# Kernel tuning notes

Measured on AMD Instinct MI355X. Metric: run time of the kernel, lower is better.

Reference implementation:

```python
import jax, jax.numpy as jnp
import numpy as np

B, T, D, C = 2, 2048, 1024, 10
F = D // 2 + 1  # rfft bins; permutations act on frequency bins (perm_freq=True)


def setup_inputs() -> dict:
    key = jax.random.key(0)
    ks = jax.random.split(key, 6)
    s = 1.0 / np.sqrt(D)
    x = jax.random.normal(ks[0], (B, T, D), jnp.float32)
    Wq = jax.random.normal(ks[1], (D, D), jnp.float32) * s
    Wk = jax.random.normal(ks[2], (D, D), jnp.float32) * s
    Wv = jax.random.normal(ks[3], (D, D), jnp.float32) * s
    Wo = jax.random.normal(ks[4], (D, D), jnp.float32) * s
    # buffer: torch.randn(C, F).argsort(-1) -> random permutations of freq bins
    perms = jnp.argsort(jax.random.normal(ks[5], (C, F)), axis=-1)
    return {"x": x, "Wq": Wq, "Wk": Wk, "Wv": Wv, "Wo": Wo, "perms": perms}


def reference(x, Wq, Wk, Wv, Wo, perms):
    # linear projections (nn.Linear applies x @ W.T)
    q = x @ Wq.T
    k = x @ Wk.T
    v = x @ Wv.T
    # HRR bind/unbind in rfft frequency domain
    fq = jnp.fft.rfft(q, axis=-1)  # (B,T,F) complex
    fk = jnp.fft.rfft(k, axis=-1)
    fv = jnp.fft.rfft(v, axis=-1)
    # gather permuted redundant copies of freq bins: (B,T,C,F) -> (C,B,T,F)
    fkp = jnp.moveaxis(fk[..., perms], 2, 0)
    fqp = jnp.moveaxis(fq[..., perms], 2, 0)
    # causal associative memory: cumulative sum of key*value bindings over time
    kv = jnp.cumsum(fkp * fv[None], axis=-2)  # (C,B,T,F)
    # unbind with query (circular correlation = multiply by conj), mean copies
    r = jnp.mean(kv * jnp.conj(fqp), axis=0)  # (B,T,F)
    values_hat = jnp.fft.irfft(r, n=D, axis=-1)  # (B,T,D)
    return values_hat @ Wo.T
```

## Files before the change

### kernel.cpp

```cpp
#include <hip/hip_runtime.h>
#include <math.h>

#define B_   2
#define T_   2048
#define D_   1024
#define C_   10
#define F_   513
#define NTOK (B_ * T_)
#define LF   3078
#define LFP  3136
#define KP2  1056
#define NCH  128
#define TC   (T_ / NCH)

typedef unsigned short us16;
typedef __attribute__((ext_vector_type(8))) __bf16 bf16x8;
typedef __attribute__((ext_vector_type(4))) float  f32x4;

#define O_XBF    ((size_t)0)
#define O_PREP   ((size_t)8388608)
#define O_WT     (O_PREP)
#define O_WOBF   (O_PREP + 6291456)
#define O_TCS    (O_PREP + 8388608)
#define O_RCAT   (O_PREP)
#define O_SFB    (O_PREP + 10489856)
#define O_MALLB  (O_SFB + 2162688)
#define O_MOUTB  (O_MALLB + 6303744)
#define O_FALL   (O_MOUTB + 2162688)
#define O_SSCAN  (O_FALL + 25690112)

__device__ __forceinline__ us16 f2b(float f) {
    union { float f; unsigned u; } v; v.f = f;
    unsigned r = v.u + 0x7FFFu + ((v.u >> 16) & 1u);
    return (us16)(r >> 16);
}

__device__ __forceinline__ float2 b2f2(unsigned w) {
    union { unsigned u; float f; } a, b;
    a.u = (w & 0xffffu) << 16;
    b.u = w & 0xffff0000u;
    return make_float2(a.f, b.f);
}

__device__ __forceinline__ void gl_lds16(const us16* g, us16* l) {
    __builtin_amdgcn_global_load_lds(
        (const __attribute__((address_space(1))) unsigned*)g,
        (__attribute__((address_space(3))) unsigned*)l, 16, 0, 0);
}

__global__ __launch_bounds__(256)
void hrr_prep(const float* __restrict__ x,  const float* __restrict__ Wq,
              const float* __restrict__ Wk, const float* __restrict__ Wv,
              const float* __restrict__ Wo,
              us16* __restrict__ Xbf, us16* __restrict__ WT,
              us16* __restrict__ WoBf, us16* __restrict__ Tcs,
              us16* __restrict__ Sfb) {
    __shared__ float t[32][33];
    const int bid = blockIdx.x, tid = threadIdx.x;
    if (bid < 4096) {
        int i = bid * 256 + tid;
        float4 v = ((const float4*)x)[i];
        ushort4 o;
        o.x = f2b(v.x); o.y = f2b(v.y); o.z = f2b(v.z); o.w = f2b(v.w);
        ((ushort4*)Xbf)[i] = o;
    } else if (bid < 5120) {
        int i = (bid - 4096) * 256 + tid;
        float4 v = ((const float4*)Wo)[i];
        ushort4 o;
        o.x = f2b(v.x); o.y = f2b(v.y); o.z = f2b(v.z); o.w = f2b(v.w);
        ((ushort4*)WoBf)[i] = o;
    } else if (bid < 8192) {
        const int l  = bid - 5120;
        const int bz = l >> 10, l2 = l & 1023;
        const int bx = (l2 & 31) * 32, by = (l2 >> 5) * 32;
        const float* W = (bz == 0) ? Wq : (bz == 1) ? Wk : Wv;
        us16* O = WT + (size_t)bz * D_ * D_;
        const int tx = tid & 31, ty = tid >> 5;
#pragma unroll
        for (int i = 0; i < 32; i += 8)
            t[ty + i][tx] = W[(size_t)(by + ty + i) * D_ + bx + tx];
        __syncthreads();
#pragma unroll
        for (int i = 0; i < 32; i += 8)
            O[(size_t)(bx + ty + i) * D_ + by + tx] = f2b(t[tx][ty + i]);
    } else if (bid < 12296) {
        int idx = (bid - 8192) * 256 + tid;
        int r = idx >> 10, e = idx & 1023;
        int f = r >> 1;
        float ang = (float)((f * e) & 1023) * 6.135923151542565e-3f;
        Tcs[idx] = f2b((r & 1) ? -sinf(ang) : cosf(ang));
    } else {
        int idx = (bid - 12296) * 256 + tid;
        int r = idx >> 10, e = idx & 1023;
        float v = 0.f;
        if (r < 1026) {
            int f = r >> 1;
            float s = (f == 0 || f == 512) ? (1.0f / 1024.0f) : (2.0f / 1024.0f);
            float ang = (float)((f * e) & 1023) * 6.135923151542565e-3f;
            v = (r & 1) ? -s * sinf(ang) : s * cosf(ang);
        }
        Sfb[idx] = f2b(v);
    }
}

template <bool OUT_BF16>
__device__ __forceinline__ void gemm_core(
    const us16* __restrict__ A, const us16* __restrict__ B, void* __restrict__ Cv,
    int M, int N, int K, int lda, int ldb, int ldc, int Ncap,
    int bm, int bn, us16* smem) {
    us16* As = smem;
    us16* Bs = smem + 8192;

    const int tid  = threadIdx.x;
    const int lane = tid & 63;
    const int wave = tid >> 6;
    const int wm = (wave >> 1) * 64;
    const int wn = (wave & 1) * 64;

    const int r0    = tid >> 2;
    const int g_lds = tid & 3;
    const int g_src = g_lds ^ ((r0 >> 1) & 3);
    const int c4    = g_src * 8;

    int rA0 = bm + r0;      if (rA0 >= M) rA0 = M - 1;
    int rA1 = bm + 64 + r0; if (rA1 >= M) rA1 = M - 1;
    int rB0 = bn + r0;      if (rB0 >= N) rB0 = N - 1;
    int rB1 = bn + 64 + r0; if (rB1 >= N) rB1 = N - 1;
    const us16* pA0 = A + (size_t)rA0 * lda + c4;
    const us16* pA1 = A + (size_t)rA1 * lda + c4;
    const us16* pB0 = B + (size_t)rB0 * ldb + c4;
    const us16* pB1 = B + (size_t)rB1 * ldb + c4;

    f32x4 acc[4][4];
#pragma unroll
    for (int i = 0; i < 4; i++)
#pragma unroll
        for (int j = 0; j < 4; j++) acc[i][j] = (f32x4){0.f, 0.f, 0.f, 0.f};

    const int fr = lane & 15;
    const int gq = ((lane >> 4) ^ ((fr >> 1) & 3)) * 8;

    const int wb = wave * 512;
#define STAGE_TILE(buf, ko)                                  \
    do {                                                     \
        us16* a_ = As + (buf) * 4096 + wb;                   \
        us16* b_ = Bs + (buf) * 4096 + wb;                   \
        gl_lds16(pA0 + (ko), a_);                            \
        gl_lds16(pA1 + (ko), a_ + 2048);                     \
        gl_lds16(pB0 + (ko), b_);                            \
        gl_lds16(pB1 + (ko), b_ + 2048);                     \
    } while (0)

    STAGE_TILE(0, 0);
    __syncthreads();

    int cur = 0;
    for (int k0 = 0; k0 < K; k0 += 32) {
        const int kn = k0 + 32;
        if (kn < K) STAGE_TILE(cur ^ 1, kn);

        const us16* Ac = As + cur * 4096;
        const us16* Bc = Bs + cur * 4096;
        bf16x8 af[4], bfr[4];
#pragma unroll
        for (int i = 0; i < 4; i++)
            af[i] = *(const bf16x8*)(Ac + (wm + i * 16 + fr) * 32 + gq);
#pragma unroll
        for (int j = 0; j < 4; j++)
            bfr[j] = *(const bf16x8*)(Bc + (wn + j * 16 + fr) * 32 + gq);
#pragma unroll
        for (int i = 0; i < 4; i++)
#pragma unroll
            for (int j = 0; j < 4; j++)
                acc[i][j] = __builtin_amdgcn_mfma_f32_16x16x32_bf16(bfr[j], af[i], acc[i][j], 0, 0, 0);

        __syncthreads();
        cur ^= 1;
    }
#undef STAGE_TILE

    const int cl  = lane & 15;
    const int rq  = (lane >> 4) * 4;
    float* lbuf = (float*)smem;
#pragma unroll
    for (int p = 0; p < 4; ++p) {
        __syncthreads();
        if ((wave >> 1) == (p >> 1)) {
            const int ib = (p & 1) * 2;
#pragma unroll
            for (int ii = 0; ii < 2; ++ii) {
                const int rl = ii * 16 + cl;
#pragma unroll
                for (int j = 0; j < 4; ++j)
                    *(f32x4*)(lbuf + rl * 132 + wn + j * 16 + rq) = acc[ib + ii][j];
            }
        }
        __syncthreads();
        const int rbase = bm + p * 32;
        if (OUT_BF16) {
            us16* C = (us16*)Cv;
#pragma unroll
            for (int rr = 0; rr < 2; ++rr) {
                const int idx = rr * 2048 + tid * 8;
                const int row = idx >> 7, col = idx & 127;
                const int grow = rbase + row, gcol = bn + col;
                if (grow < M && gcol + 8 <= Ncap) {
                    const float* s = lbuf + row * 132 + col;
                    uint4 o;
                    o.x = (unsigned)f2b(s[0]) | ((unsigned)f2b(s[1]) << 16);
                    o.y = (unsigned)f2b(s[2]) | ((unsigned)f2b(s[3]) << 16);
                    o.z = (unsigned)f2b(s[4]) | ((unsigned)f2b(s[5]) << 16);
                    o.w = (unsigned)f2b(s[6]) | ((unsigned)f2b(s[7]) << 16);
                    *(uint4*)(C + (size_t)grow * ldc + gcol) = o;
                }
            }
        } else {
            float* C = (float*)Cv;
#pragma unroll
            for (int rr = 0; rr < 4; ++rr) {
                const int idx = rr * 1024 + tid * 4;
                const int row = idx >> 7, col = idx & 127;
                const int grow = rbase + row, gcol = bn + col;
                if (grow < M && gcol + 4 <= Ncap)
                    *(float4*)(C + (size_t)grow * ldc + gcol) =
                        *(const float4*)(lbuf + row * 132 + col);
            }
        }
    }
}

template <bool OUT_BF16>
__global__ __launch_bounds__(256, 3)
void hrr_gemm(const us16* __restrict__ A, const us16* __restrict__ B,
              void* __restrict__ C, int M, int N, int K,
              int lda, int ldb, int ldc, int Ncap, int swz) {
    __shared__ us16 smem[16384];
    int bx = blockIdx.x, by = blockIdx.y;
    if (swz) {
        const int gx = gridDim.x;
        const int id = bx + gx * by;
        const int q = (gx * gridDim.y) >> 3;
        const int nid = (id & 7) * q + (id >> 3);
        bx = nid % gx; by = nid / gx;
    }
    gemm_core<OUT_BF16>(A, B, C, M, N, K, lda, ldb, ldc, Ncap,
                        by * 128, bx * 128, smem);
}

__global__ __launch_bounds__(256, 3)
void hrr_gemm_builders(const us16* __restrict__ Tcs, const us16* __restrict__ WT,
                       us16* __restrict__ MallB, const us16* __restrict__ WoBf,
                       const us16* __restrict__ Sfb, us16* __restrict__ MoutB) {
    __shared__ us16 smem[16384];
    const int bm = blockIdx.y * 128, bn = blockIdx.x * 128;
    const int z = blockIdx.z;
    if (z < 3)
        gemm_core<true>(Tcs, WT + (size_t)z * D_ * D_,
                        MallB + (size_t)z * 1026 * 1024,
                        1026, 1024, 1024, 1024, 1024, 1024, 1024, bm, bn, smem);
    else
        gemm_core<true>(WoBf, Sfb, MoutB,
                        1024, KP2, 1024, 1024, 1024, KP2, KP2, bm, bn, smem);
}

__global__ __launch_bounds__(512, 2)
void hrr_gemm_main(const us16* __restrict__ A, const us16* __restrict__ B,
                   us16* __restrict__ C) {
    __shared__ us16 smem[65536];
    us16* Asb = smem;
    us16* Bsb = smem + 32768;

    const int tid  = threadIdx.x;
    const int lane = tid & 63;
    const int wave = tid >> 6;

    int id = blockIdx.x + 13 * blockIdx.y;
    id = (id & 7) * 26 + (id >> 3);
    const int bx = id % 13, by = id / 13;
    const int bm = by * 256, bn = bx * 256;

    const int srow = tid >> 3;
    const int sgr  = (tid & 7) ^ (srow & 7);
    const us16* gA[4];
    const us16* gB[4];
#pragma unroll
    for (int g = 0; g < 4; ++g) {
        int ra = bm + g * 64 + srow; if (ra > NTOK - 1) ra = NTOK - 1;
        int rb = bn + g * 64 + srow; if (rb > LF - 1)   rb = LF - 1;
        gA[g] = A + (size_t)ra * 1024 + sgr * 8;
        gB[g] = B + (size_t)rb * 1024 + sgr * 8;
    }

    f32x4 acc[8][4];
#pragma unroll
    for (int i = 0; i < 8; i++)
#pragma unroll
        for (int j = 0; j < 4; j++) acc[i][j] = (f32x4){0.f, 0.f, 0.f, 0.f};

    const int wmw = (wave >> 2) * 128;
    const int wnw = (wave & 3) * 64;
    const int fr  = lane & 15;
    const int gr  = lane >> 4;
    const int l7  = lane & 7;

#define STAGE3(buf, ko)                                            \
    do {                                                           \
        us16* a_ = Asb + (buf) * 16384 + wave * 512;               \
        us16* b_ = Bsb + (buf) * 16384 + wave * 512;               \
        gl_lds16(gA[0] + (ko), a_);                                \
        gl_lds16(gA[1] + (ko), a_ + 4096);                         \
        gl_lds16(gA[2] + (ko), a_ + 8192);                         \
        gl_lds16(gA[3] + (ko), a_ + 12288);                        \
        gl_lds16(gB[0] + (ko), b_);                                \
        gl_lds16(gB[1] + (ko), b_ + 4096);                         \
        gl_lds16(gB[2] + (ko), b_ + 8192);                         \
        gl_lds16(gB[3] + (ko), b_ + 12288);                        \
    } while (0)

#define RBAR                                                       \
    do {                                                           \
        asm volatile("" ::: "memory");                             \
        __builtin_amdgcn_s_barrier();                              \
        asm volatile("" ::: "memory");                             \
    } while (0)

#define LOAD_A(ih)                                                              \
    do {                                                                        \
        _Pragma("unroll")                                                       \
        for (int i = 0; i < 4; ++i)                                             \
            _Pragma("unroll")                                                   \
            for (int ks = 0; ks < 2; ++ks)                                      \
                af[i][ks] = *(const bf16x8*)(Ac +                               \
                    (wmw + (ih) * 64 + i * 16 + fr) * 64 +                      \
                    (((ks << 2) | gr) ^ l7) * 8);                               \
    } while (0)

#define LOAD_B(jh)                                                              \
    do {                                                                        \
        _Pragma("unroll")                                                       \
        for (int j = 0; j < 2; ++j)                                             \
            _Pragma("unroll")                                                   \
            for (int ks = 0; ks < 2; ++ks)                                      \
                bfr[j][ks] = *(const bf16x8*)(Bc +                              \
                    (wnw + (jh) * 32 + j * 16 + fr) * 64 +                      \
                    (((ks << 2) | gr) ^ l7) * 8);                               \
    } while (0)

#define MFMA_Q(ih, jh)                                                          \
    do {                                                                        \
        __builtin_amdgcn_s_setprio(1);                                          \
        _Pragma("unroll")                                                       \
        for (int i = 0; i < 4; ++i)                                             \
            _Pragma("unroll")                                                   \
            for (int j = 0; j < 2; ++j)                                         \
                _Pragma("unroll")                                               \
                for (int ks = 0; ks < 2; ++ks)                                  \
                    acc[(ih) * 4 + i][(jh) * 2 + j] =                           \
                        __builtin_amdgcn_mfma_f32_16x16x32_bf16(                \
                            bfr[j][ks], af[i][ks],                              \
                            acc[(ih) * 4 + i][(jh) * 2 + j], 0, 0, 0);          \
        __builtin_amdgcn_s_setprio(0);                                          \
    } while (0)

    STAGE3(0, 0);
    asm volatile("s_waitcnt vmcnt(0)" ::: "memory");
    __builtin_amdgcn_s_barrier();
    asm volatile("" ::: "memory");

    int cur = 0;
#pragma unroll 1
    for (int t = 0; t < 16; ++t) {
        if (t < 15) STAGE3(cur ^ 1, (t + 1) * 64);

        const us16* Ac = Asb + cur * 16384;
        const us16* Bc = Bsb + cur * 16384;
        bf16x8 af[4][2], bfr[2][2];

        LOAD_A(0); LOAD_B(0); MFMA_Q(0, 0); RBAR;
        LOAD_B(1);            MFMA_Q(0, 1); RBAR;
        LOAD_A(1);            MFMA_Q(1, 1); RBAR;
        LOAD_B(0);            MFMA_Q(1, 0);
        asm volatile("s_waitcnt vmcnt(0)" ::: "memory");
        __builtin_amdgcn_s_barrier();
        asm volatile("" ::: "memory");
        cur ^= 1;
    }
#undef STAGE3
#undef LOAD_A
#undef LOAD_B
#undef MFMA_Q
#undef RBAR

    __syncthreads();
    float* lw = (float*)smem + wave * (32 * 68);
    const int cl = lane & 15;
    const int rq = (lane >> 4) * 4;
#pragma unroll
    for (int p = 0; p < 4; ++p) {
#pragma unroll
        for (int ii = 0; ii < 2; ++ii) {
            const int ifr = p * 2 + ii;
#pragma unroll
            for (int j = 0; j < 4; ++j)
                *(f32x4*)(lw + (ii * 16 + cl) * 68 + j * 16 + rq) = acc[ifr][j];
        }
        __syncthreads();
#pragma unroll
        for (int rr = 0; rr < 4; ++rr) {
            const int idx = rr * 512 + lane * 8;
            const int row = idx >> 6, col = idx & 63;
            const int grow = bm + wmw + p * 32 + row;
            const int gcol = bn + wnw + col;
            if (gcol + 8 <= LFP) {
                const float* s = lw + row * 68 + col;
                uint4 o;
                o.x = (unsigned)f2b(s[0]) | ((unsigned)f2b(s[1]) << 16);
                o.y = (unsigned)f2b(s[2]) | ((unsigned)f2b(s[3]) << 16);
                o.z = (unsigned)f2b(s[4]) | ((unsigned)f2b(s[5]) << 16);
                o.w = (unsigned)f2b(s[6]) | ((unsigned)f2b(s[7]) << 16);
                *(uint4*)(C + (size_t)grow * LFP + gcol) = o;
            }
        }
        __syncthreads();
    }
}

__global__ __launch_bounds__(256, 4)
void hrr_scan_sums(const us16* __restrict__ Fall, const int* __restrict__ perms,
                   float* __restrict__ S) {
    const int n = blockIdx.x, b = blockIdx.y, half = blockIdx.z;
    const int tid = threadIdx.x;
    const int f0 = half * 256;
    __shared__ float2 kc[F_], vc[257];

    float aR[2][C_], aI[2][C_];
    int gg[2][C_];
#pragma unroll
    for (int i = 0; i < 2; i++) {
        const int f = (i == 0) ? (f0 + tid) : 512;
        const bool act = (i == 0) || (half == 1 && tid == 0);
#pragma unroll
        for (int c = 0; c < C_; c++) {
            gg[i][c] = act ? perms[c * F_ + f] : 0;
            aR[i][c] = aI[i][c] = 0.f;
        }
    }

    const unsigned* rowb =
        (const unsigned*)(Fall + (size_t)(b * T_ + n * TC) * LFP);
    const int R32 = LFP / 2;

    unsigned rk0, rk1, rk2 = 0, rv0, rv1 = 0;
#define SFETCH(tl)                                                   \
    do {                                                             \
        const unsigned* r_ = rowb + (size_t)(tl) * R32;              \
        rk0 = r_[513 + tid];                                         \
        rk1 = r_[769 + tid];                                         \
        rv0 = r_[1026 + f0 + tid];                                   \
        if (tid == 0) { rk2 = r_[1025]; rv1 = r_[1538]; }            \
    } while (0)

    SFETCH(0);
    for (int tl = 0; tl < TC; tl++) {
        __syncthreads();
        kc[tid]       = b2f2(rk0);
        kc[256 + tid] = b2f2(rk1);
        vc[tid]       = b2f2(rv0);
        if (tid == 0) { kc[512] = b2f2(rk2); if (half) vc[256] = b2f2(rv1); }
        __syncthreads();
        if (tl + 1 < TC) SFETCH(tl + 1);
#pragma unroll
        for (int i = 0; i < 2; i++) {
            const int lv = (i == 0) ? tid : 256;
            if (i == 0 || (half == 1 && tid == 0)) {
                float2 v = vc[lv];
#pragma unroll
                for (int c = 0; c < C_; c++) {
                    float2 k = kc[gg[i][c]];
                    aR[i][c] += k.x * v.x - k.y * v.y;
                    aI[i][c] += k.x * v.y + k.y * v.x;
                }
            }
        }
    }
#undef SFETCH
#pragma unroll
    for (int i = 0; i < 2; i++) {
        const int f = (i == 0) ? (f0 + tid) : 512;
        if (i == 0 || (half == 1 && tid == 0)) {
#pragma unroll
            for (int c = 0; c < C_; c++) {
                size_t a = ((((size_t)c * B_ + b) * NCH + n) * F_ + f) * 2;
                S[a] = aR[i][c]; S[a + 1] = aI[i][c];
            }
        }
    }
}

__global__ void hrr_scan_prefix(float* __restrict__ S) {
    int tid = blockIdx.x * 256 + threadIdx.x;
    if (tid >= C_ * B_ * F_) return;
    int c = tid / (B_ * F_);
    int r = tid % (B_ * F_);
    int b = r / F_, f = r % F_;
    size_t base = (((size_t)c * B_ + b) * NCH) * F_ + f;
    float runR = 0.f, runI = 0.f;
    for (int n0 = 0; n0 < NCH; n0 += 8) {
        float tR[8], tI[8];
#pragma unroll
        for (int u = 0; u < 8; u++) {
            size_t a = (base + (size_t)(n0 + u) * F_) * 2;
            tR[u] = S[a]; tI[u] = S[a + 1];
        }
#pragma unroll
        for (int u = 0; u < 8; u++) {
            size_t a = (base + (size_t)(n0 + u) * F_) * 2;
            S[a] = runR; S[a + 1] = runI;
            runR += tR[u]; runI += tI[u];
        }
    }
}

__global__ __launch_bounds__(256, 4)
void hrr_scan_apply(const us16* __restrict__ Fall, const int* __restrict__ perms,
                    const float* __restrict__ S, us16* __restrict__ Rcat) {
    const int n = blockIdx.x, b = blockIdx.y, half = blockIdx.z;
    const int tid = threadIdx.x;
    const int f0 = half * 256;
    __shared__ float2 qc[F_], kc[F_], vc[257];

    float kvR[2][C_], kvI[2][C_];
    int gg[2][C_];
#pragma unroll
    for (int i = 0; i < 2; i++) {
        const int f = (i == 0) ? (f0 + tid) : 512;
        const bool act = (i == 0) || (half == 1 && tid == 0);
#pragma unroll
        for (int c = 0; c < C_; c++) {
            gg[i][c] = act ? perms[c * F_ + f] : 0;
            if (act) {
                size_t a = ((((size_t)c * B_ + b) * NCH + n) * F_ + f) * 2;
                kvR[i][c] = S[a]; kvI[i][c] = S[a + 1];
            } else { kvR[i][c] = 0.f; kvI[i][c] = 0.f; }
        }
    }

    const unsigned* rowb =
        (const unsigned*)(Fall + (size_t)(b * T_ + n * TC) * LFP);
    const int R32 = LFP / 2;

    unsigned rq0, rq1, rq2 = 0, rk0, rk1, rk2 = 0, rv0, rv1 = 0;
#define AFETCH(tl)                                                   \
    do {                                                             \
        const unsigned* r_ = rowb + (size_t)(tl) * R32;              \
        rq0 = r_[tid];       rq1 = r_[256 + tid];                    \
        rk0 = r_[513 + tid]; rk1 = r_[769 + tid];                    \
        rv0 = r_[1026 + f0 + tid];                                   \
        if (tid == 0) { rq2 = r_[512]; rk2 = r_[1025]; rv1 = r_[1538]; } \
    } while (0)

    AFETCH(0);
    for (int tl = 0; tl < TC; tl++) {
        const int tt = b * T_ + n * TC + tl;
        __syncthreads();
        qc[tid]       = b2f2(rq0);
        qc[256 + tid] = b2f2(rq1);
        kc[tid]       = b2f2(rk0);
        kc[256 + tid] = b2f2(rk1);
        vc[tid]       = b2f2(rv0);
        if (tid == 0) {
            qc[512] = b2f2(rq2); kc[512] = b2f2(rk2);
            if (half) vc[256] = b2f2(rv1);
        }
        __syncthreads();
        if (tl + 1 < TC) AFETCH(tl + 1);
        unsigned* out32 = (unsigned*)(Rcat + (size_t)tt * KP2);
#pragma unroll
        for (int i = 0; i < 2; i++) {
            const int f = (i == 0) ? (f0 + tid) : 512;
            const int lv = (i == 0) ? tid : 256;
            if (i == 0 || (half == 1 && tid == 0)) {
                float2 v = vc[lv];
                float accR = 0.f, accI = 0.f;
#pragma unroll
                for (int c = 0; c < C_; c++) {
                    int g = gg[i][c];
                    float2 k = kc[g];
                    float nR = kvR[i][c] + k.x * v.x - k.y * v.y;
                    float nI = kvI[i][c] + k.x * v.y + k.y * v.x;
                    kvR[i][c] = nR; kvI[i][c] = nI;
                    float2 q = qc[g];
                    accR += nR * q.x + nI * q.y;
                    accI += nI * q.x - nR * q.y;
                }
                out32[f] = (unsigned)f2b(accR * 0.1f)
                         | ((unsigned)f2b(accI * 0.1f) << 16);
            }
        }
        if (half == 0 && tid < 15)
            out32[513 + tid] = 0;
    }
#undef AFETCH
}

extern "C" void kernel_launch(void* const* d_in, const int* in_sizes, int n_in,
                              void* d_out, int out_size, void* d_ws, size_t ws_size,
                              hipStream_t stream) {
    const float* x  = (const float*)d_in[0];
    const float* Wq = (const float*)d_in[1];
    const float* Wk = (const float*)d_in[2];
    const float* Wv = (const float*)d_in[3];
    const float* Wo = (const float*)d_in[4];
    const int* perms = (const int*)d_in[5];
    float* out = (float*)d_out;

    char* ws = (char*)d_ws;
    us16* Xbf   = (us16*)(ws + O_XBF);
    us16* WT    = (us16*)(ws + O_WT);
    us16* WoBf  = (us16*)(ws + O_WOBF);
    us16* Tcs   = (us16*)(ws + O_TCS);
    us16* Sfb   = (us16*)(ws + O_SFB);
    us16* MallB = (us16*)(ws + O_MALLB);
    us16* MoutB = (us16*)(ws + O_MOUTB);
    us16* Rcat  = (us16*)(ws + O_RCAT);
    us16* Fall  = (us16*)(ws + O_FALL);
    float* Ssc  = (float*)(ws + O_SSCAN);

    hrr_prep<<<16520, 256, 0, stream>>>(x, Wq, Wk, Wv, Wo, Xbf, WT, WoBf, Tcs, Sfb);

    hrr_gemm_builders<<<dim3(9, 9, 4), 256, 0, stream>>>(Tcs, WT, MallB, WoBf, Sfb, MoutB);

    hrr_gemm_main<<<dim3(13, 16), 512, 0, stream>>>(Xbf, MallB, Fall);

    hrr_scan_sums<<<dim3(NCH, B_, 2), 256, 0, stream>>>(Fall, perms, Ssc);
    hrr_scan_prefix<<<(C_ * B_ * F_ + 255) / 256, 256, 0, stream>>>(Ssc);
    hrr_scan_apply<<<dim3(NCH, B_, 2), 256, 0, stream>>>(Fall, perms, Ssc, Rcat);

    hrr_gemm<false><<<dim3(8, 32), 256, 0, stream>>>(
        Rcat, MoutB, out, NTOK, D_, KP2, KP2, KP2, D_, D_, 1);
}
```

Measured before the change: 217.2 us.

## Shrink shared GEMM tiles to 128x64 and merge DFT basis generation

Replaces the 128x128 GEMM core with a 128x64 variant used by the builder GEMMs and the final output projection. This doubles block counts to fill more CUs and raises the occupancy hint from 3 to 4. The prep kernel now writes the forward and scaled inverse DFT basis tables in one pass using fast __sinf/__cosf intrinsics, and only zero-fills the padding rows of the inverse table. In exchange, each B tile is reused less, and the fast intrinsics are slightly less accurate, though the results are rounded to bf16 anyway.

Result: no change. 214.5 us (-1.2%).

```diff
diff --git a/kernel.cpp b/kernel.cpp
--- a/kernel.cpp
+++ b/kernel.cpp
@@ -88,23 +88,18 @@
         int r = idx >> 10, e = idx & 1023;
         int f = r >> 1;
         float ang = (float)((f * e) & 1023) * 6.135923151542565e-3f;
-        Tcs[idx] = f2b((r & 1) ? -sinf(ang) : cosf(ang));
+        float val = (r & 1) ? -__sinf(ang) : __cosf(ang);
+        float s = (f == 0 || f == 512) ? (1.0f / 1024.0f) : (2.0f / 1024.0f);
+        Tcs[idx] = f2b(val);
+        Sfb[idx] = f2b(s * val);
     } else {
-        int idx = (bid - 12296) * 256 + tid;
-        int r = idx >> 10, e = idx & 1023;
-        float v = 0.f;
-        if (r < 1026) {
-            int f = r >> 1;
-            float s = (f == 0 || f == 512) ? (1.0f / 1024.0f) : (2.0f / 1024.0f);
-            float ang = (float)((f * e) & 1023) * 6.135923151542565e-3f;
-            v = (r & 1) ? -s * sinf(ang) : s * cosf(ang);
-        }
-        Sfb[idx] = f2b(v);
+        int idx2 = (bid - 12296) * 256 + tid;
+        Sfb[1026 * 1024 + idx2] = 0;
     }
 }
 
 template <bool OUT_BF16>
-__device__ __forceinline__ void gemm_core(
+__device__ __forceinline__ void gemm_core64(
     const us16* __restrict__ A, const us16* __restrict__ B, void* __restrict__ Cv,
     int M, int N, int K, int lda, int ldb, int ldc, int Ncap,
     int bm, int bn, us16* smem) {
@@ -114,8 +109,7 @@
     const int tid  = threadIdx.x;
     const int lane = tid & 63;
     const int wave = tid >> 6;
-    const int wm = (wave >> 1) * 64;
-    const int wn = (wave & 1) * 64;
+    const int wm = wave * 32;
 
     const int r0    = tid >> 2;
     const int g_lds = tid & 3;
@@ -125,15 +119,13 @@
     int rA0 = bm + r0;      if (rA0 >= M) rA0 = M - 1;
     int rA1 = bm + 64 + r0; if (rA1 >= M) rA1 = M - 1;
     int rB0 = bn + r0;      if (rB0 >= N) rB0 = N - 1;
-    int rB1 = bn + 64 + r0; if (rB1 >= N) rB1 = N - 1;
     const us16* pA0 = A + (size_t)rA0 * lda + c4;
     const us16* pA1 = A + (size_t)rA1 * lda + c4;
     const us16* pB0 = B + (size_t)rB0 * ldb + c4;
-    const us16* pB1 = B + (size_t)rB1 * ldb + c4;
-
-    f32x4 acc[4][4];
-#pragma unroll
-    for (int i = 0; i < 4; i++)
+
+    f32x4 acc[2][4];
+#pragma unroll
+    for (int i = 0; i < 2; i++)
 #pragma unroll
         for (int j = 0; j < 4; j++) acc[i][j] = (f32x4){0.f, 0.f, 0.f, 0.f};
 
@@ -144,11 +136,10 @@
 #define STAGE_TILE(buf, ko)                                  \
     do {                                                     \
         us16* a_ = As + (buf) * 4096 + wb;                   \
-        us16* b_ = Bs + (buf) * 4096 + wb;                   \
+        us16* b_ = Bs + (buf) * 2048 + wb;                   \
         gl_lds16(pA0 + (ko), a_);                            \
         gl_lds16(pA1 + (ko), a_ + 2048);                     \
         gl_lds16(pB0 + (ko), b_);                            \
-        gl_lds16(pB1 + (ko), b_ + 2048);                     \
     } while (0)
 
     STAGE_TILE(0, 0);
@@ -160,16 +151,16 @@
         if (kn < K) STAGE_TILE(cur ^ 1, kn);
 
         const us16* Ac = As + cur * 4096;
-        const us16* Bc = Bs + cur * 4096;
-        bf16x8 af[4], bfr[4];
-#pragma unroll
-        for (int i = 0; i < 4; i++)
+        const us16* Bc = Bs + cur * 2048;
+        bf16x8 af[2], bfr[4];
+#pragma unroll
+        for (int i = 0; i < 2; i++)
             af[i] = *(const bf16x8*)(Ac + (wm + i * 16 + fr) * 32 + gq);
 #pragma unroll
         for (int j = 0; j < 4; j++)
-            bfr[j] = *(const bf16x8*)(Bc + (wn + j * 16 + fr) * 32 + gq);
-#pragma unroll
-        for (int i = 0; i < 4; i++)
+            bfr[j] = *(const bf16x8*)(Bc + (j * 16 + fr) * 32 + gq);
+#pragma unroll
+        for (int i = 0; i < 2; i++)
 #pragma unroll
             for (int j = 0; j < 4; j++)
                 acc[i][j] = __builtin_amdgcn_mfma_f32_16x16x32_bf16(bfr[j], af[i], acc[i][j], 0, 0, 0);
@@ -185,56 +176,51 @@
 #pragma unroll
     for (int p = 0; p < 4; ++p) {
         __syncthreads();
-        if ((wave >> 1) == (p >> 1)) {
-            const int ib = (p & 1) * 2;
-#pragma unroll
-            for (int ii = 0; ii < 2; ++ii) {
-                const int rl = ii * 16 + cl;
+        if (wave == p) {
+#pragma unroll
+            for (int i = 0; i < 2; ++i) {
+                const int rl = i * 16 + cl;
 #pragma unroll
                 for (int j = 0; j < 4; ++j)
-                    *(f32x4*)(lbuf + rl * 132 + wn + j * 16 + rq) = acc[ib + ii][j];
+                    *(f32x4*)(lbuf + rl * 68 + j * 16 + rq) = acc[i][j];
             }
         }
         __syncthreads();
         const int rbase = bm + p * 32;
         if (OUT_BF16) {
             us16* C = (us16*)Cv;
-#pragma unroll
-            for (int rr = 0; rr < 2; ++rr) {
-                const int idx = rr * 2048 + tid * 8;
-                const int row = idx >> 7, col = idx & 127;
-                const int grow = rbase + row, gcol = bn + col;
-                if (grow < M && gcol + 8 <= Ncap) {
-                    const float* s = lbuf + row * 132 + col;
-                    uint4 o;
-                    o.x = (unsigned)f2b(s[0]) | ((unsigned)f2b(s[1]) << 16);
-                    o.y = (unsigned)f2b(s[2]) | ((unsigned)f2b(s[3]) << 16);
-                    o.z = (unsigned)f2b(s[4]) | ((unsigned)f2b(s[5]) << 16);
-                    o.w = (unsigned)f2b(s[6]) | ((unsigned)f2b(s[7]) << 16);
-                    *(uint4*)(C + (size_t)grow * ldc + gcol) = o;
-                }
+            const int row = tid >> 3, col = (tid * 8) & 63;
+            const int grow = rbase + row, gcol = bn + col;
+            if (grow < M && gcol + 8 <= Ncap) {
+                const float* s = lbuf + row * 68 + col;
+                uint4 o;
+                o.x = (unsigned)f2b(s[0]) | ((unsigned)f2b(s[1]) << 16);
+                o.y = (unsigned)f2b(s[2]) | ((unsigned)f2b(s[3]) << 16);
+                o.z = (unsigned)f2b(s[4]) | ((unsigned)f2b(s[5]) << 16);
+                o.w = (unsigned)f2b(s[6]) | ((unsigned)f2b(s[7]) << 16);
+                *(uint4*)(C + (size_t)grow * ldc + gcol) = o;
             }
         } else {
             float* C = (float*)Cv;
 #pragma unroll
-            for (int rr = 0; rr < 4; ++rr) {
+            for (int rr = 0; rr < 2; ++rr) {
                 const int idx = rr * 1024 + tid * 4;
-                const int row = idx >> 7, col = idx & 127;
+                const int row = idx >> 6, col = idx & 63;
                 const int grow = rbase + row, gcol = bn + col;
                 if (grow < M && gcol + 4 <= Ncap)
                     *(float4*)(C + (size_t)grow * ldc + gcol) =
-                        *(const float4*)(lbuf + row * 132 + col);
+                        *(const float4*)(lbuf + row * 68 + col);
             }
         }
     }
 }
 
 template <bool OUT_BF16>
-__global__ __launch_bounds__(256, 3)
+__global__ __launch_bounds__(256, 4)
 void hrr_gemm(const us16* __restrict__ A, const us16* __restrict__ B,
               void* __restrict__ C, int M, int N, int K,
               int lda, int ldb, int ldc, int Ncap, int swz) {
-    __shared__ us16 smem[16384];
+    __shared__ us16 smem[12288];
     int bx = blockIdx.x, by = blockIdx.y;
     if (swz) {
         const int gx = gridDim.x;
@@ -243,24 +229,28 @@
         const int nid = (id & 7) * q + (id >> 3);
         bx = nid % gx; by = nid / gx;
     }
-    gemm_core<OUT_BF16>(A, B, C, M, N, K, lda, ldb, ldc, Ncap,
-                        by * 128, bx * 128, smem);
-}
-
-__global__ __launch_bounds__(256, 3)
+    gemm_core64<OUT_BF16>(A, B, C, M, N, K, lda, ldb, ldc, Ncap,
+                          by * 128, bx * 64, smem);
+}
+
+__global__ __launch_bounds__(256, 4)
 void hrr_gemm_builders(const us16* __restrict__ Tcs, const us16* __restrict__ WT,
                        us16* __restrict__ MallB, const us16* __restrict__ WoBf,
                        const us16* __restrict__ Sfb, us16* __restrict__ MoutB) {
-    __shared__ us16 smem[16384];
-    const int bm = blockIdx.y * 128, bn = blockIdx.x * 128;
+    __shared__ us16 smem[12288];
     const int z = blockIdx.z;
-    if (z < 3)
-        gemm_core<true>(Tcs, WT + (size_t)z * D_ * D_,
-                        MallB + (size_t)z * 1026 * 1024,
-                        1026, 1024, 1024, 1024, 1024, 1024, 1024, bm, bn, smem);
-    else
-        gemm_core<true>(WoBf, Sfb, MoutB,
-                        1024, KP2, 1024, 1024, 1024, KP2, KP2, bm, bn, smem);
+    if (z < 3) {
+        if (blockIdx.x >= 16) return;
+        gemm_core64<true>(Tcs, WT + (size_t)z * D_ * D_,
+                          MallB + (size_t)z * 1026 * 1024,
+                          1026, 1024, 1024, 1024, 1024, 1024, 1024,
+                          blockIdx.y * 128, blockIdx.x * 64, smem);
+    } else {
+        if (blockIdx.y >= 8) return;
+        gemm_core64<true>(WoBf, Sfb, MoutB,
+                          1024, KP2, 1024, 1024, 1024, KP2, KP2,
+                          blockIdx.y * 128, blockIdx.x * 64, smem);
+    }
 }
 
 __global__ __launch_bounds__(512, 2)
@@ -626,9 +616,9 @@
     us16* Fall  = (us16*)(ws + O_FALL);
     float* Ssc  = (float*)(ws + O_SSCAN);
 
-    hrr_prep<<<16520, 256, 0, stream>>>(x, Wq, Wk, Wv, Wo, Xbf, WT, WoBf, Tcs, Sfb);
-
-    hrr_gemm_builders<<<dim3(9, 9, 4), 256, 0, stream>>>(Tcs, WT, MallB, WoBf, Sfb, MoutB);
+    hrr_prep<<<12416, 256, 0, stream>>>(x, Wq, Wk, Wv, Wo, Xbf, WT, WoBf, Tcs, Sfb);
+
+    hrr_gemm_builders<<<dim3(17, 9, 4), 256, 0, stream>>>(Tcs, WT, MallB, WoBf, Sfb, MoutB);
 
     hrr_gemm_main<<<dim3(13, 16), 512, 0, stream>>>(Xbf, MallB, Fall);
 
@@ -636,6 +626,6 @@
     hrr_scan_prefix<<<(C_ * B_ * F_ + 255) / 256, 256, 0, stream>>>(Ssc);
     hrr_scan_apply<<<dim3(NCH, B_, 2), 256, 0, stream>>>(Fall, perms, Ssc, Rcat);
 
-    hrr_gemm<false><<<dim3(8, 32), 256, 0, stream>>>(
+    hrr_gemm<false><<<dim3(16, 32), 256, 0, stream>>>(
         Rcat, MoutB, out, NTOK, D_, KP2, KP2, KP2, D_, D_, 1);
 }
```
